# Kernel tuning notes

Hardware: AMD Instinct MI355X
Metric: run time of the kernel (lower is better)

The kernel has to match this reference:

```python
import jax, jax.numpy as jnp
import numpy as np

C = 256
NUM_HEADS = 8
GROUPS = 8
EPS = 1e-5


def setup_inputs() -> dict:
    key = jax.random.key(0)
    ks = jax.random.split(key, 7)
    B, H, W = 2, 64, 64
    x = jax.random.normal(ks[0], (B, C, H, W), dtype=jnp.float32)
    gn_weight = jnp.ones((C,), dtype=jnp.float32)
    gn_bias = jnp.zeros((C,), dtype=jnp.float32)
    # 1x1 convs == per-pixel linear layers
    w_qkv = jax.random.normal(ks[1], (3 * C, C), dtype=jnp.float32) * (1.0 / np.sqrt(C))
    b_qkv = jax.random.normal(ks[2], (3 * C,), dtype=jnp.float32) * 0.01
    w_proj = jax.random.normal(ks[3], (C, C), dtype=jnp.float32) * (1.0 / np.sqrt(C))
    b_proj = jax.random.normal(ks[4], (C,), dtype=jnp.float32) * 0.01
    return {"x": x, "gn_weight": gn_weight, "gn_bias": gn_bias,
            "w_qkv": w_qkv, "b_qkv": b_qkv, "w_proj": w_proj, "b_proj": b_proj}


def reference(x, gn_weight, gn_bias, w_qkv, b_qkv, w_proj, b_proj):
    B, Cc, H, W = x.shape
    nh = NUM_HEADS
    hd = Cc // nh
    N = H * W
    scale = hd ** (-0.5)

    # GroupNorm(8, C): normalize over (C/G, H, W) per group, biased variance
    xg = x.reshape(B, GROUPS, Cc // GROUPS, H, W)
    mean = xg.mean(axis=(2, 3, 4), keepdims=True)
    var = xg.var(axis=(2, 3, 4), keepdims=True)
    hn = (xg - mean) * jax.lax.rsqrt(var + EPS)
    hn = hn.reshape(B, Cc, H, W) * gn_weight[None, :, None, None] + gn_bias[None, :, None, None]

    hf = hn.reshape(B, Cc, N)                       # [B, C, N]
    qkv = jnp.einsum('oc,bcn->bon', w_qkv, hf) + b_qkv[None, :, None]  # [B, 3C, N]
    qkv = qkv.reshape(B, 3, nh, hd, N)
    # q,k,v: [B, nh, N, hd]
    q = jnp.transpose(qkv[:, 0], (0, 1, 3, 2))
    k = jnp.transpose(qkv[:, 1], (0, 1, 3, 2))
    v = jnp.transpose(qkv[:, 2], (0, 1, 3, 2))

    attn = jnp.einsum('bhqd,bhkd->bhqk', q, k) * scale  # [B, nh, N, N]
    attn = jax.nn.softmax(attn, axis=-1)
    o = jnp.einsum('bhqk,bhkd->bhqd', attn, v)           # [B, nh, N, hd]
    o = jnp.transpose(o, (0, 1, 3, 2)).reshape(B, Cc, H, W)

    of = o.reshape(B, Cc, N)
    out = jnp.einsum('oc,bcn->bon', w_proj, of) + b_proj[None, :, None]
    return out.reshape(B, Cc, H, W)
```

## Files before the change

### kernel.cpp

```cpp
#include <hip/hip_runtime.h>


typedef _Float16 half8 __attribute__((ext_vector_type(8)));
typedef __fp16   fp16x2 __attribute__((ext_vector_type(2)));
typedef float    f32x4 __attribute__((ext_vector_type(4)));
typedef int      int2v __attribute__((ext_vector_type(2)));
typedef int      int4v __attribute__((ext_vector_type(4)));

__device__ __forceinline__ f32x4 mfma16(half8 a, half8 b, f32x4 c) {
  return __builtin_amdgcn_mfma_f32_16x16x32_f16(a, b, c, 0, 0, 0);
}

#if __has_builtin(__builtin_amdgcn_exp2f)
#define EXP2(x) __builtin_amdgcn_exp2f(x)
#else
#define EXP2(x) exp2f(x)
#endif

__device__ __forceinline__ unsigned short h_bits(_Float16 h) {
  return __builtin_bit_cast(unsigned short, h);
}
__device__ __forceinline__ int h2_bits(fp16x2 h) {
  return __builtin_bit_cast(int, h);
}

__device__ __forceinline__ half8 cvt8(const float* p) {
  f32x4 v0 = *(const f32x4*)p;
  f32x4 v1 = *(const f32x4*)(p + 4);
  half8 h;
#pragma unroll
  for (int j = 0; j < 4; ++j) { h[j] = (_Float16)v0[j]; h[4 + j] = (_Float16)v1[j]; }
  return h;
}

__device__ __forceinline__ void gl16(const _Float16* g, _Float16* l) {
  __builtin_amdgcn_global_load_lds(
      (const __attribute__((address_space(1))) unsigned int*)g,
      (__attribute__((address_space(3))) unsigned int*)l, 16, 0, 0);
}

constexpr float CSCALE = (float)(1.4426950408889634 / 5.656854249492381);

__global__ __launch_bounds__(256) void gn_stats(const float* __restrict__ x,
                                                float* __restrict__ stats) {
  const int bg = blockIdx.x, ch = blockIdx.y, tid = threadIdx.x;
  const float* p = x + (size_t)bg * 131072 + (size_t)ch * 4096;
  float s = 0.f, ss = 0.f;
#pragma unroll
  for (int j = 0; j < 4; ++j) {
    f32x4 v = *(const f32x4*)(p + j * 1024 + tid * 4);
#pragma unroll
    for (int k = 0; k < 4; ++k) { s += v[k]; ss += v[k] * v[k]; }
  }
#pragma unroll
  for (int m = 1; m <= 32; m <<= 1) { s += __shfl_xor(s, m); ss += __shfl_xor(ss, m); }
  __shared__ float red[8];
  const int wv = tid >> 6;
  if ((tid & 63) == 0) { red[wv * 2] = s; red[wv * 2 + 1] = ss; }
  __syncthreads();
  if (tid == 0) {
    float S = red[0] + red[2] + red[4] + red[6];
    float SS = red[1] + red[3] + red[5] + red[7];
    stats[(bg * 32 + ch) * 2] = S;
    stats[(bg * 32 + ch) * 2 + 1] = SS;
  }
}

__global__ __launch_bounds__(256) void gn_apply(const float* __restrict__ x,
                                                const float* __restrict__ gw,
                                                const float* __restrict__ gb,
                                                const float* __restrict__ stats,
                                                _Float16* __restrict__ hn) {
  __shared__ float tile[64 * 65];
  __shared__ float mv[2][2];
  const int tid = threadIdx.x;
  const int a = tid & 15;
  const int row16 = tid >> 4;
  const int b = blockIdx.z, c0 = blockIdx.y * 64, n0 = blockIdx.x * 64;
  if (tid < 2) {
    const int g = (c0 >> 5) + tid;
    const int bg = b * 8 + g;
    float S = 0.f, SS = 0.f;
    for (int ch = 0; ch < 32; ++ch) {
      S += stats[(bg * 32 + ch) * 2];
      SS += stats[(bg * 32 + ch) * 2 + 1];
    }
    const float mean = S * (1.f / 131072.f);
    const float var = SS * (1.f / 131072.f) - mean * mean;
    mv[tid][0] = mean;
    mv[tid][1] = rsqrtf(var + 1e-5f);
  }
  __syncthreads();
#pragma unroll
  for (int m = 0; m < 4; ++m) {
    const int cl = row16 + 16 * m;
    const int c = c0 + cl;
    const float mean = mv[cl >> 5][0];
    const float rstd = mv[cl >> 5][1];
    const float ga = gw[c] * rstd;
    const float be = gb[c] - mean * ga;
    f32x4 xv = *(const f32x4*)(x + ((size_t)(b * 256 + c)) * 4096 + n0 + a * 4);
#pragma unroll
    for (int j = 0; j < 4; ++j) tile[cl * 65 + a * 4 + j] = xv[j] * ga + be;
  }
  __syncthreads();
#pragma unroll
  for (int m = 0; m < 4; ++m) {
    const int nl = row16 + 16 * m;
    const int cb = a * 4;
    int2v uh;
    unsigned short hh[4];
#pragma unroll
    for (int j = 0; j < 4; ++j) {
      hh[j] = h_bits((_Float16)tile[(cb + j) * 65 + nl]);
    }
    uh[0] = hh[0] | (hh[1] << 16); uh[1] = hh[2] | (hh[3] << 16);
    size_t off = ((size_t)(b * 4096 + n0 + nl)) * 256 + c0 + cb;
    *(int2v*)(hn + off) = uh;
  }
}

template <int MODE, int BN>
__global__ __launch_bounds__(256) void gemm_f16(
    const float* __restrict__ Wf, const _Float16* __restrict__ Bm,
    const float* __restrict__ bias,
    _Float16* __restrict__ qkT, _Float16* __restrict__ v_t,
    float* __restrict__ outp) {
  constexpr int RB = BN / 32;
  constexpr int NT = BN / 16;
  __shared__ _Float16 a_lds[2][4096];
  __shared__ _Float16 b_lds[2][BN * 64];
  const int tid = threadIdx.x, lane = tid & 63, wv = tid >> 6;
  const int qq = lane >> 4, ii = lane & 15;
  const int m0 = blockIdx.x * 64, n0 = blockIdx.y * BN, bz = blockIdx.z;

  const float* asrc[2];
  int dsta[2];
#pragma unroll
  for (int rep = 0; rep < 2; ++rep) {
    const int idx = tid + 256 * rep;
    dsta[rep] = idx * 8;
    const int j = idx >> 7, c = (idx >> 6) & 1, l = idx & 63;
    const int lq = l >> 4, li = l & 15;
    asrc[rep] = Wf + (size_t)(m0 + 16 * j + li) * 256 + 32 * c + 8 * lq;
  }
  const _Float16* bsrc[RB];
  int dstb[RB];
#pragma unroll
  for (int rep = 0; rep < RB; ++rep) {
    const int idx = tid + 256 * rep;
    dstb[rep] = idx * 8;
    const int j = idx >> 7, c = (idx >> 6) & 1, l = idx & 63;
    const int lq = l >> 4, li = l & 15;
    bsrc[rep] = Bm + ((size_t)(bz * 4096 + n0 + 16 * j + li)) * 256 + 32 * c + 8 * lq;
  }

  f32x4 acc[NT] = {};

  half8 ar[2], br[RB];
#pragma unroll
  for (int rep = 0; rep < 2; ++rep) ar[rep] = cvt8(asrc[rep]);
#pragma unroll
  for (int rep = 0; rep < RB; ++rep) br[rep] = *(const half8*)bsrc[rep];
#pragma unroll
  for (int rep = 0; rep < 2; ++rep) *(half8*)(a_lds[0] + dsta[rep]) = ar[rep];
#pragma unroll
  for (int rep = 0; rep < RB; ++rep) *(half8*)(b_lds[0] + dstb[rep]) = br[rep];
  __syncthreads();

  for (int it = 0; it < 4; ++it) {
    const int cur = it & 1;
    if (it < 3) {
      const int ko = (it + 1) * 64;
#pragma unroll
      for (int rep = 0; rep < 2; ++rep) ar[rep] = cvt8(asrc[rep] + ko);
#pragma unroll
      for (int rep = 0; rep < RB; ++rep) br[rep] = *(const half8*)(bsrc[rep] + ko);
    }
    half8 ah0 = *(const half8*)(a_lds[cur] + ((wv * 2 + 0) * 64 + lane) * 8);
    half8 ah1 = *(const half8*)(a_lds[cur] + ((wv * 2 + 1) * 64 + lane) * 8);
#pragma unroll
    for (int t = 0; t < NT; ++t) {
      half8 b0 = *(const half8*)(b_lds[cur] + ((t * 2 + 0) * 64 + lane) * 8);
      half8 b1 = *(const half8*)(b_lds[cur] + ((t * 2 + 1) * 64 + lane) * 8);
      acc[t] = mfma16(ah0, b0, acc[t]);
      acc[t] = mfma16(ah1, b1, acc[t]);
    }
    if (it < 3) {
      _Float16* an = a_lds[cur ^ 1];
      _Float16* bn = b_lds[cur ^ 1];
#pragma unroll
      for (int rep = 0; rep < 2; ++rep) *(half8*)(an + dsta[rep]) = ar[rep];
#pragma unroll
      for (int rep = 0; rep < RB; ++rep) *(half8*)(bn + dstb[rep]) = br[rep];
    }
    __syncthreads();
  }

  const int och0 = m0 + 16 * wv + 4 * qq;
  if (MODE == 0) {
    if (m0 < 512) {
      const float sc = (m0 < 256) ? CSCALE : 1.0f;
#pragma unroll
      for (int t = 0; t < NT; ++t) {
        const int n = n0 + 16 * t + ii;
        unsigned short hh[4];
#pragma unroll
        for (int r = 0; r < 4; ++r) {
          hh[r] = h_bits((_Float16)((acc[t][r] + bias[och0 + r]) * sc));
        }
        int2v u;
        u[0] = hh[0] | (hh[1] << 16);
        u[1] = hh[2] | (hh[3] << 16);
        *(int2v*)(qkT + ((size_t)(bz * 4096 + n)) * 512 + och0) = u;
      }
    } else {
#pragma unroll
      for (int t = 0; t < NT; ++t) {
#pragma unroll
        for (int r = 0; r < 4; ++r) {
          const int och = och0 + r;
          const int d = och - 512;
          const int hd_ = d & 31, head = d >> 5;
          const int n = n0 + 16 * t + ii;
          v_t[((size_t)((bz * 8 + head) * 32 + hd_)) * 4096 + n] =
              (_Float16)(acc[t][r] + bias[och]);
        }
      }
    }
  } else {
#pragma unroll
    for (int t = 0; t < NT; ++t) {
#pragma unroll
      for (int r = 0; r < 4; ++r) {
        const int och = och0 + r;
        const int n = n0 + 16 * t + ii;
        outp[((size_t)(bz * 256 + och)) * 4096 + n] = acc[t][r] + bias[och];
      }
    }
  }
}

__global__ __launch_bounds__(512) void attn_kernel(
    const _Float16* __restrict__ qkT, const _Float16* __restrict__ v_t,
    float* __restrict__ opart, float* __restrict__ lpart, int nkb) {
  __shared__ _Float16 k_lds[2][4096];
  __shared__ _Float16 v_lds[2][4096];
  const int tid = threadIdx.x, lane = tid & 63, wv = tid >> 6;
  const int qq = lane >> 4, ii = lane & 15;
  const int bh = blockIdx.y, b = bh >> 3, h = bh & 7;
  const int n0 = blockIdx.x * 256;
  const int part = blockIdx.z;
  const int key0 = part * (nkb * 128);

  const _Float16* qbase =
      qkT + ((size_t)(b * 4096 + n0 + 32 * wv + ii)) * 512 + h * 32 + 8 * qq;
  half8 qf0 = *(const half8*)qbase;
  half8 qf1 = *(const half8*)(qbase + (size_t)16 * 512);

  const int f = tid >> 6, l = tid & 63;
  const int fq = l >> 4, fi = l & 15;
  const int su = f >> 1, shf = f & 1;
  const int g = 32 * su + 4 * shf + 8 * (fi >> 2) + (fi & 3);
  const _Float16* ksrc =
      qkT + ((size_t)(b * 4096 + key0 + g)) * 512 + 256 + h * 32 + 8 * fq;
  const _Float16* vsrc =
      v_t + ((size_t)(bh * 32 + 16 * shf + fi)) * 4096 + key0 + 32 * su + 8 * fq;
  const int wb = wv * 512;

  half8 ones8;
#pragma unroll
  for (int j = 0; j < 8; ++j) ones8[j] = (_Float16)1.0f;

  f32x4 o00 = {}, o10 = {}, o01 = {}, o11 = {}, accl0 = {}, accl1 = {};

  gl16(ksrc, &k_lds[0][wb]);
  gl16(vsrc, &v_lds[0][wb]);

  for (int kb = 0; kb < nkb; ++kb) {
    const int cur = kb & 1;
    asm volatile("s_waitcnt vmcnt(0)" ::: "memory");
    __builtin_amdgcn_s_barrier();
    if (kb + 1 < nkb) {
      gl16(ksrc + (size_t)(kb + 1) * 65536, &k_lds[cur ^ 1][wb]);
      gl16(vsrc + (size_t)(kb + 1) * 128, &v_lds[cur ^ 1][wb]);
    }
    __builtin_amdgcn_sched_barrier(0);

    const _Float16* kbase = k_lds[cur];
    const _Float16* vbase = v_lds[cur];
#pragma unroll
    for (int u = 0; u < 4; ++u) {
      half8 kfa = *(const half8*)(kbase + u * 1024 + lane * 8);
      half8 kfb = *(const half8*)(kbase + u * 1024 + 512 + lane * 8);
      f32x4 z = {};
      f32x4 sa0 = mfma16(kfa, qf0, z);
      f32x4 sb0 = mfma16(kfb, qf0, z);
      f32x4 sa1 = mfma16(kfa, qf1, z);
      f32x4 sb1 = mfma16(kfb, qf1, z);
      int4v p0, p1;
      p0[0] = h2_bits(__builtin_amdgcn_cvt_pkrtz(EXP2(sa0[0]), EXP2(sa0[1])));
      p0[1] = h2_bits(__builtin_amdgcn_cvt_pkrtz(EXP2(sa0[2]), EXP2(sa0[3])));
      p0[2] = h2_bits(__builtin_amdgcn_cvt_pkrtz(EXP2(sb0[0]), EXP2(sb0[1])));
      p0[3] = h2_bits(__builtin_amdgcn_cvt_pkrtz(EXP2(sb0[2]), EXP2(sb0[3])));
      p1[0] = h2_bits(__builtin_amdgcn_cvt_pkrtz(EXP2(sa1[0]), EXP2(sa1[1])));
      p1[1] = h2_bits(__builtin_amdgcn_cvt_pkrtz(EXP2(sa1[2]), EXP2(sa1[3])));
      p1[2] = h2_bits(__builtin_amdgcn_cvt_pkrtz(EXP2(sb1[0]), EXP2(sb1[1])));
      p1[3] = h2_bits(__builtin_amdgcn_cvt_pkrtz(EXP2(sb1[2]), EXP2(sb1[3])));
      half8 pt0 = __builtin_bit_cast(half8, p0);
      half8 pt1 = __builtin_bit_cast(half8, p1);
      half8 vf0 = *(const half8*)(vbase + u * 1024 + lane * 8);
      half8 vf1 = *(const half8*)(vbase + u * 1024 + 512 + lane * 8);
      o00 = mfma16(vf0, pt0, o00);
      o10 = mfma16(vf1, pt0, o10);
      accl0 = mfma16(ones8, pt0, accl0);
      o01 = mfma16(vf0, pt1, o01);
      o11 = mfma16(vf1, pt1, o11);
      accl1 = mfma16(ones8, pt1, accl1);
    }
  }

#pragma unroll
  for (int hf = 0; hf < 2; ++hf) {
    const f32x4 oa = hf ? o01 : o00;
    const f32x4 ob = hf ? o11 : o10;
    const int q = n0 + 32 * wv + 16 * hf + ii;
    float* base = opart + ((size_t)((part * 2 + b) * 4096 + q)) * 256 + h * 32;
    *(f32x4*)(base + 4 * qq) = oa;
    *(f32x4*)(base + 16 + 4 * qq) = ob;
    if (qq == 0) {
      lpart[((size_t)((part * 2 + b) * 4096 + q)) * 8 + h] = hf ? accl1[0] : accl0[0];
    }
  }
}

__global__ __launch_bounds__(256) void attn_combine(
    const float* __restrict__ opart, const float* __restrict__ lpart,
    _Float16* __restrict__ o16, int parts) {
  const int t = threadIdx.x;
  const int cq = (t & 63) * 4;
  const int kr = t >> 6;
  const int row = blockIdx.x * 4 + kr;
  const int b = row >> 12;
  const int q = row & 4095;
  const int hh = cq >> 5;
  f32x4 O = {};
  float L = 0.f;
  for (int p = 0; p < parts; ++p) {
    const size_t rbase = ((size_t)((p * 2 + b) * 4096 + q));
    O += *(const f32x4*)(opart + rbase * 256 + cq);
    L += lpart[rbase * 8 + hh];
  }
  const float inv = 1.0f / L;
  unsigned short hw[4];
#pragma unroll
  for (int j = 0; j < 4; ++j) hw[j] = h_bits((_Float16)(O[j] * inv));
  int2v u;
  u[0] = hw[0] | (hw[1] << 16);
  u[1] = hw[2] | (hw[3] << 16);
  *(int2v*)(o16 + (size_t)row * 256 + cq) = u;
}

extern "C" void kernel_launch(void* const* d_in, const int* in_sizes, int n_in,
                              void* d_out, int out_size, void* d_ws, size_t ws_size,
                              hipStream_t stream) {
  const float* x     = (const float*)d_in[0];
  const float* gnw   = (const float*)d_in[1];
  const float* gnb   = (const float*)d_in[2];
  const float* wqkv  = (const float*)d_in[3];
  const float* bqkv  = (const float*)d_in[4];
  const float* wproj = (const float*)d_in[5];
  const float* bproj = (const float*)d_in[6];
  float* out = (float*)d_out;

  char* ws = (char*)d_ws;
  size_t off = 0;
  auto alloc = [&](size_t bytes) -> char* {
    char* p = ws + off;
    off += (bytes + 255) & ~(size_t)255;
    return p;
  };
  float*    stats  = (float*)alloc((size_t)16 * 32 * 2 * 4);
  _Float16* hn     = (_Float16*)alloc((size_t)2 * 4096 * 256 * 2);
  _Float16* qkT    = (_Float16*)alloc((size_t)2 * 4096 * 512 * 2);
  _Float16* v_t    = (_Float16*)alloc((size_t)16 * 32 * 4096 * 2);

  int parts = 4;
  {
    const size_t need4 = (size_t)8 * 4096 * 256 * 4 + (size_t)8 * 4096 * 8 * 4 + 1024;
    if (off + need4 > ws_size) parts = 2;
  }
  float*    opart  = (float*)alloc((size_t)(parts * 2) * 4096 * 256 * 4);
  float*    lpart  = (float*)alloc((size_t)(parts * 2) * 4096 * 8 * 4);
  _Float16* o16 = hn;
  if (off > ws_size) return;

  gn_stats<<<dim3(16, 32), 256, 0, stream>>>(x, stats);
  gn_apply<<<dim3(64, 4, 2), 256, 0, stream>>>(x, gnw, gnb, stats, hn);
  gemm_f16<0, 128><<<dim3(12, 32, 2), 256, 0, stream>>>(wqkv, hn, bqkv, qkT,
                                                        v_t, nullptr);
  const int nkb = 4096 / parts / 128;
  attn_kernel<<<dim3(16, 16, parts), 512, 0, stream>>>(qkT, v_t, opart, lpart,
                                                       nkb);
  attn_combine<<<2048, 256, 0, stream>>>(opart, lpart, o16, parts);
  gemm_f16<1, 64><<<dim3(4, 64, 2), 256, 0, stream>>>(wproj, o16, bproj,
                                                      nullptr, nullptr, out);
}
```

Before: 151.7 us.

## Fuse GroupNorm apply into QKV GEMM B-operand loads

Removes the separate gn_apply kernel and its fp16 hn intermediate. The QKV GEMM now reads x in fp32 straight from the NCHW layout, applies the per-channel GroupNorm scale and shift from shared memory, and converts to fp16 while loading B tiles. This saves one launch and a write/read round trip of the normalized activations. In exchange each B element becomes a strided scalar fp32 load (stride 4096 across channels, coalesced across n), and every one of the 12 M-blocks re-reads x and redoes the normalization, so the GEMM's global traffic and per-load work go up.

```diff
diff --git a/kernel.cpp b/kernel.cpp
--- a/kernel.cpp
+++ b/kernel.cpp
@@ -66,63 +66,11 @@
   }
 }
 
-__global__ __launch_bounds__(256) void gn_apply(const float* __restrict__ x,
-                                                const float* __restrict__ gw,
-                                                const float* __restrict__ gb,
-                                                const float* __restrict__ stats,
-                                                _Float16* __restrict__ hn) {
-  __shared__ float tile[64 * 65];
-  __shared__ float mv[2][2];
-  const int tid = threadIdx.x;
-  const int a = tid & 15;
-  const int row16 = tid >> 4;
-  const int b = blockIdx.z, c0 = blockIdx.y * 64, n0 = blockIdx.x * 64;
-  if (tid < 2) {
-    const int g = (c0 >> 5) + tid;
-    const int bg = b * 8 + g;
-    float S = 0.f, SS = 0.f;
-    for (int ch = 0; ch < 32; ++ch) {
-      S += stats[(bg * 32 + ch) * 2];
-      SS += stats[(bg * 32 + ch) * 2 + 1];
-    }
-    const float mean = S * (1.f / 131072.f);
-    const float var = SS * (1.f / 131072.f) - mean * mean;
-    mv[tid][0] = mean;
-    mv[tid][1] = rsqrtf(var + 1e-5f);
-  }
-  __syncthreads();
-#pragma unroll
-  for (int m = 0; m < 4; ++m) {
-    const int cl = row16 + 16 * m;
-    const int c = c0 + cl;
-    const float mean = mv[cl >> 5][0];
-    const float rstd = mv[cl >> 5][1];
-    const float ga = gw[c] * rstd;
-    const float be = gb[c] - mean * ga;
-    f32x4 xv = *(const f32x4*)(x + ((size_t)(b * 256 + c)) * 4096 + n0 + a * 4);
-#pragma unroll
-    for (int j = 0; j < 4; ++j) tile[cl * 65 + a * 4 + j] = xv[j] * ga + be;
-  }
-  __syncthreads();
-#pragma unroll
-  for (int m = 0; m < 4; ++m) {
-    const int nl = row16 + 16 * m;
-    const int cb = a * 4;
-    int2v uh;
-    unsigned short hh[4];
-#pragma unroll
-    for (int j = 0; j < 4; ++j) {
-      hh[j] = h_bits((_Float16)tile[(cb + j) * 65 + nl]);
-    }
-    uh[0] = hh[0] | (hh[1] << 16); uh[1] = hh[2] | (hh[3] << 16);
-    size_t off = ((size_t)(b * 4096 + n0 + nl)) * 256 + c0 + cb;
-    *(int2v*)(hn + off) = uh;
-  }
-}
-
 template <int MODE, int BN>
 __global__ __launch_bounds__(256) void gemm_f16(
     const float* __restrict__ Wf, const _Float16* __restrict__ Bm,
+    const float* __restrict__ xf, const float* __restrict__ gw,
+    const float* __restrict__ gb, const float* __restrict__ stats,
     const float* __restrict__ bias,
     _Float16* __restrict__ qkT, _Float16* __restrict__ v_t,
     float* __restrict__ outp) {
@@ -130,6 +78,8 @@
   constexpr int NT = BN / 16;
   __shared__ _Float16 a_lds[2][4096];
   __shared__ _Float16 b_lds[2][BN * 64];
+  __shared__ float2 gab[MODE == 0 ? 256 : 1];
+  __shared__ float mvm[8], mvr[8];
   const int tid = threadIdx.x, lane = tid & 63, wv = tid >> 6;
   const int qq = lane >> 4, ii = lane & 15;
   const int m0 = blockIdx.x * 64, n0 = blockIdx.y * BN, bz = blockIdx.z;
@@ -145,6 +95,8 @@
     asrc[rep] = Wf + (size_t)(m0 + 16 * j + li) * 256 + 32 * c + 8 * lq;
   }
   const _Float16* bsrc[RB];
+  const float* xsrc[RB];
+  int cb0[RB];
   int dstb[RB];
 #pragma unroll
   for (int rep = 0; rep < RB; ++rep) {
@@ -152,8 +104,54 @@
     dstb[rep] = idx * 8;
     const int j = idx >> 7, c = (idx >> 6) & 1, l = idx & 63;
     const int lq = l >> 4, li = l & 15;
-    bsrc[rep] = Bm + ((size_t)(bz * 4096 + n0 + 16 * j + li)) * 256 + 32 * c + 8 * lq;
-  }
+    const int n = n0 + 16 * j + li;
+    if constexpr (MODE == 0) {
+      cb0[rep] = 32 * c + 8 * lq;
+      xsrc[rep] = xf + ((size_t)(bz * 256 + cb0[rep])) * 4096 + n;
+    } else {
+      bsrc[rep] = Bm + ((size_t)(bz * 4096 + n)) * 256 + 32 * c + 8 * lq;
+    }
+  }
+
+  if constexpr (MODE == 0) {
+    if (tid < 8) {
+      const int bg = bz * 8 + tid;
+      float S = 0.f, SS = 0.f;
+      for (int ch = 0; ch < 32; ++ch) {
+        S += stats[(bg * 32 + ch) * 2];
+        SS += stats[(bg * 32 + ch) * 2 + 1];
+      }
+      const float mean = S * (1.f / 131072.f);
+      const float var = SS * (1.f / 131072.f) - mean * mean;
+      mvm[tid] = mean;
+      mvr[tid] = rsqrtf(var + 1e-5f);
+    }
+    __syncthreads();
+    {
+      const int c = tid;
+      const int g = c >> 5;
+      const float ga = gw[c] * mvr[g];
+      const float be = gb[c] - mvm[g] * ga;
+      gab[c] = make_float2(ga, be);
+    }
+    __syncthreads();
+  }
+
+  auto fetchB = [&](int rep, int it) -> half8 {
+    half8 h;
+    if constexpr (MODE == 0) {
+      const float* p = xsrc[rep] + (size_t)it * 64 * 4096;
+      const int cb = it * 64 + cb0[rep];
+#pragma unroll
+      for (int i = 0; i < 8; ++i) {
+        const float2 ab = gab[cb + i];
+        h[i] = (_Float16)(p[(size_t)i * 4096] * ab.x + ab.y);
+      }
+    } else {
+      h = *(const half8*)(bsrc[rep] + it * 64);
+    }
+    return h;
+  };
 
   f32x4 acc[NT] = {};
 
@@ -161,7 +159,7 @@
 #pragma unroll
   for (int rep = 0; rep < 2; ++rep) ar[rep] = cvt8(asrc[rep]);
 #pragma unroll
-  for (int rep = 0; rep < RB; ++rep) br[rep] = *(const half8*)bsrc[rep];
+  for (int rep = 0; rep < RB; ++rep) br[rep] = fetchB(rep, 0);
 #pragma unroll
   for (int rep = 0; rep < 2; ++rep) *(half8*)(a_lds[0] + dsta[rep]) = ar[rep];
 #pragma unroll
@@ -175,7 +173,7 @@
 #pragma unroll
       for (int rep = 0; rep < 2; ++rep) ar[rep] = cvt8(asrc[rep] + ko);
 #pragma unroll
-      for (int rep = 0; rep < RB; ++rep) br[rep] = *(const half8*)(bsrc[rep] + ko);
+      for (int rep = 0; rep < RB; ++rep) br[rep] = fetchB(rep, it + 1);
     }
     half8 ah0 = *(const half8*)(a_lds[cur] + ((wv * 2 + 0) * 64 + lane) * 8);
     half8 ah1 = *(const half8*)(a_lds[cur] + ((wv * 2 + 1) * 64 + lane) * 8);
@@ -381,7 +379,7 @@
     return p;
   };
   float*    stats  = (float*)alloc((size_t)16 * 32 * 2 * 4);
-  _Float16* hn     = (_Float16*)alloc((size_t)2 * 4096 * 256 * 2);
+  _Float16* o16    = (_Float16*)alloc((size_t)2 * 4096 * 256 * 2);
   _Float16* qkT    = (_Float16*)alloc((size_t)2 * 4096 * 512 * 2);
   _Float16* v_t    = (_Float16*)alloc((size_t)16 * 32 * 4096 * 2);
 
@@ -392,17 +390,16 @@
   }
   float*    opart  = (float*)alloc((size_t)(parts * 2) * 4096 * 256 * 4);
   float*    lpart  = (float*)alloc((size_t)(parts * 2) * 4096 * 8 * 4);
-  _Float16* o16 = hn;
   if (off > ws_size) return;
 
   gn_stats<<<dim3(16, 32), 256, 0, stream>>>(x, stats);
-  gn_apply<<<dim3(64, 4, 2), 256, 0, stream>>>(x, gnw, gnb, stats, hn);
-  gemm_f16<0, 128><<<dim3(12, 32, 2), 256, 0, stream>>>(wqkv, hn, bqkv, qkT,
-                                                        v_t, nullptr);
+  gemm_f16<0, 128><<<dim3(12, 32, 2), 256, 0, stream>>>(
+      wqkv, nullptr, x, gnw, gnb, stats, bqkv, qkT, v_t, nullptr);
   const int nkb = 4096 / parts / 128;
   attn_kernel<<<dim3(16, 16, parts), 512, 0, stream>>>(qkT, v_t, opart, lpart,
                                                        nkb);
   attn_combine<<<2048, 256, 0, stream>>>(opart, lpart, o16, parts);
-  gemm_f16<1, 64><<<dim3(4, 64, 2), 256, 0, stream>>>(wproj, o16, bproj,
-                                                      nullptr, nullptr, out);
-}
+  gemm_f16<1, 64><<<dim3(4, 64, 2), 256, 0, stream>>>(
+      wproj, o16, nullptr, nullptr, nullptr, nullptr, bproj, nullptr, nullptr,
+      out);
+}
```

Result: no change. 149.9 us (-1.2%).
